# Kernel optimization log

Measured on AMD Instinct MI355X. Metric: run time of the kernel, lower is better.

Reference implementation:

```python
import jax, jax.numpy as jnp
import numpy as np

N_NODES = 100000
DEG = 16
N_EDGES = N_NODES * DEG
D_IN = 128
D_OUT = 128


def setup_inputs() -> dict:
    key = jax.random.key(0)
    k1, k2, k3 = jax.random.split(key, 3)
    X = jax.random.normal(k1, (N_NODES, D_IN), dtype=jnp.float32)
    weights = jax.random.normal(k2, (D_IN, D_OUT), dtype=jnp.float32) * (1.0 / np.sqrt(D_OUT))
    # fixed-degree CSR: row i owns edges [i*DEG, (i+1)*DEG)
    row_pointers = (jnp.arange(N_NODES + 1, dtype=jnp.int32) * DEG)
    column_index = jax.random.randint(k3, (N_EDGES,), 0, N_NODES, dtype=jnp.int32)
    # TC-GNN kernel-scheduling metadata (no effect on math)
    blockPartition = jnp.zeros((N_NODES // DEG,), dtype=jnp.int32)
    edgeToColumn = jnp.zeros((N_EDGES,), dtype=jnp.int32)
    edgeToRow = jnp.zeros((N_EDGES,), dtype=jnp.int32)
    return {"X": X, "weights": weights, "row_pointers": row_pointers,
            "column_index": column_index, "blockPartition": blockPartition,
            "edgeToColumn": edgeToColumn, "edgeToRow": edgeToRow}


def _csr_spmm(feat, row_pointers, column_index):
    # out[i] = sum_{e in row i} feat[column_index[e]]  (unweighted SpMM)
    n = row_pointers.shape[0] - 1
    e = column_index.shape[0]
    # map each edge to its source row via searchsorted on the CSR pointer array
    row_ids = jnp.searchsorted(row_pointers, jnp.arange(e, dtype=row_pointers.dtype), side='right') - 1
    gathered = feat[column_index]  # [E, D]
    return jax.ops.segment_sum(gathered, row_ids, num_segments=n)


def reference(X, weights, row_pointers, column_index, blockPartition, edgeToColumn, edgeToRow):
    X_prime = jnp.matmul(X, weights)                      # [N, D_OUT] dense GEMM
    return _csr_spmm(X_prime, row_pointers, column_index)  # [N, D_OUT] neighbor sum
```

## Files before the change

### kernel.cpp

```cpp
#include <hip/hip_runtime.h>
#include <hip/hip_bf16.h>

#define N_NODES 100000
#define DEG 16
#define D 128

typedef __bf16 bf16x8 __attribute__((ext_vector_type(8)));
typedef float f32x4 __attribute__((ext_vector_type(4)));

__device__ __forceinline__ ushort f32_to_bf16u(float f) {
  unsigned u = __float_as_uint(f);
  u = (u + 0x7fffu + ((u >> 16) & 1u)) >> 16;
  return (ushort)u;
}

__device__ __forceinline__ int swz(int row, int k) {
  return (row << 7) + (k ^ ((row & 7) << 3));
}

__global__ void k_convW(const float* __restrict__ W, ushort* __restrict__ Wt) {
  const int t = threadIdx.x;
  for (int j = 0; j < 64; ++j) {
    int pos = (j << 8) + t;
    int k = pos >> 7, n = pos & 127;
    Wt[swz(n, k)] = f32_to_bf16u(W[pos]);
  }
}

__global__ __launch_bounds__(256, 2) void k_gemm(const float* __restrict__ X,
                                                 const ushort* __restrict__ Wt,
                                                 ushort* __restrict__ Xp) {
  __shared__ __align__(16) ushort As[128 * 128];
  __shared__ __align__(16) ushort Ws[128 * 128];
  const int tid = threadIdx.x;
  const int row0 = blockIdx.x << 7;

  {
    const uint4* src = (const uint4*)Wt;
    uint4* dst = (uint4*)Ws;
#pragma unroll
    for (int j = 0; j < 8; ++j) dst[(j << 8) + tid] = src[(j << 8) + tid];
  }
#pragma unroll
  for (int j = 0; j < 16; ++j) {
    int pos = (j << 8) + tid;
    int r = pos >> 5;
    int c4 = (pos & 31) << 2;
    int grow = row0 + r;
    float4 v = make_float4(0.f, 0.f, 0.f, 0.f);
    if (grow < N_NODES) v = *(const float4*)(X + grow * D + c4);
    ushort4 b;
    b.x = f32_to_bf16u(v.x); b.y = f32_to_bf16u(v.y);
    b.z = f32_to_bf16u(v.z); b.w = f32_to_bf16u(v.w);
    *(ushort4*)(As + swz(r, c4)) = b;
  }
  __syncthreads();

  const int wave = tid >> 6;
  const int lane = tid & 63;
  const int lhi = lane >> 4;
  const int llo = lane & 15;

  f32x4 acc[2][8];
#pragma unroll
  for (int m = 0; m < 2; ++m)
#pragma unroll
    for (int n = 0; n < 8; ++n)
      acc[m][n] = (f32x4){0.f, 0.f, 0.f, 0.f};

#pragma unroll
  for (int t = 0; t < 4; ++t) {
    const int k0 = (t << 5) + (lhi << 3);
    bf16x8 a[2], b[8];
#pragma unroll
    for (int m = 0; m < 2; ++m) {
      int r = (wave << 5) + (m << 4) + llo;
      a[m] = *(const bf16x8*)(As + swz(r, k0));
    }
#pragma unroll
    for (int n = 0; n < 8; ++n) {
      int cc = (n << 4) + llo;
      b[n] = *(const bf16x8*)(Ws + swz(cc, k0));
    }
#pragma unroll
    for (int m = 0; m < 2; ++m)
#pragma unroll
      for (int n = 0; n < 8; ++n)
        acc[m][n] = __builtin_amdgcn_mfma_f32_16x16x32_bf16(a[m], b[n], acc[m][n], 0, 0, 0);
  }

#pragma unroll
  for (int m = 0; m < 2; ++m) {
    int rbase = row0 + (wave << 5) + (m << 4) + (lhi << 2);
#pragma unroll
    for (int n = 0; n < 8; ++n) {
      int col = (n << 4) + llo;
#pragma unroll
      for (int r = 0; r < 4; ++r) {
        int grow = rbase + r;
        if (grow < N_NODES) Xp[grow * D + col] = f32_to_bf16u(acc[m][n][r]);
      }
    }
  }
}

__global__ __launch_bounds__(256) void k_spmm(const ushort* __restrict__ Xp,
                                              const int* __restrict__ ci,
                                              float* __restrict__ out) {
  const int wave = threadIdx.x >> 6;
  const int lane = threadIdx.x & 63;
  const int row = (blockIdx.x << 2) + wave;
  if (row >= N_NODES) return;

  int idx = 0;
  if (lane < DEG) idx = ci[row * DEG + lane];

  float ax = 0.f, ay = 0.f;
#pragma unroll
  for (int e = 0; e < DEG; ++e) {
    int col = __shfl(idx, e);
    unsigned v = *(const unsigned*)(Xp + col * D + (lane << 1));
    ax += __uint_as_float(v << 16);
    ay += __uint_as_float(v & 0xffff0000u);
  }
  *(float2*)(out + row * D + (lane << 1)) = make_float2(ax, ay);
}

extern "C" void kernel_launch(void* const* d_in, const int* in_sizes, int n_in,
                              void* d_out, int out_size, void* d_ws, size_t ws_size,
                              hipStream_t stream) {
  const float* X = (const float*)d_in[0];
  const float* W = (const float*)d_in[1];
  const int* ci = (const int*)d_in[3];

  ushort* Wt = (ushort*)d_ws;
  ushort* Xp = (ushort*)d_ws + 128 * 128;
  float* out = (float*)d_out;

  k_convW<<<1, 256, 0, stream>>>(W, Wt);
  k_gemm<<<(N_NODES + 127) / 128, 256, 0, stream>>>(X, Wt, Xp);
  k_spmm<<<N_NODES / 4, 256, 0, stream>>>(Xp, ci, out);
}
```

Before: 95.72 us.

## Feed GEMM A operand from registers and permute Xp layout for vector stores

The GEMM now loads X rows straight into registers and converts them to bf16 fragments in place, dropping the shared-memory A tile and its barrier traffic. It also writes Xp with a column permutation, so each lane stores a packed 16-byte vector instead of scalar halves. The SpMM kernel issues all 16 neighbour gathers before accumulating, uses nontemporal loads and stores for the index and output streams, and undoes the permutation when writing the output. The cost is that output writes become scattered scalar stores, and register pressure in the GEMM rises.

New measurement: 90.58 us. 1.06x faster.

```diff
diff --git a/kernel.cpp b/kernel.cpp
--- a/kernel.cpp
+++ b/kernel.cpp
@@ -8,10 +8,10 @@
 typedef __bf16 bf16x8 __attribute__((ext_vector_type(8)));
 typedef float f32x4 __attribute__((ext_vector_type(4)));
 
-__device__ __forceinline__ ushort f32_to_bf16u(float f) {
-  unsigned u = __float_as_uint(f);
-  u = (u + 0x7fffu + ((u >> 16) & 1u)) >> 16;
-  return (ushort)u;
+__device__ __forceinline__ unsigned pk2(float a, float b) {
+  union { __bf16 h[2]; unsigned u; } x;
+  x.h[0] = (__bf16)a; x.h[1] = (__bf16)b;
+  return x.u;
 }
 
 __device__ __forceinline__ int swz(int row, int k) {
@@ -23,17 +23,22 @@
   for (int j = 0; j < 64; ++j) {
     int pos = (j << 8) + t;
     int k = pos >> 7, n = pos & 127;
-    Wt[swz(n, k)] = f32_to_bf16u(W[pos]);
+    union { __bf16 h; ushort u; } c;
+    c.h = (__bf16)W[pos];
+    Wt[swz(n, k)] = c.u;
   }
 }
 
 __global__ __launch_bounds__(256, 2) void k_gemm(const float* __restrict__ X,
                                                  const ushort* __restrict__ Wt,
                                                  ushort* __restrict__ Xp) {
-  __shared__ __align__(16) ushort As[128 * 128];
   __shared__ __align__(16) ushort Ws[128 * 128];
   const int tid = threadIdx.x;
   const int row0 = blockIdx.x << 7;
+  const int wave = tid >> 6;
+  const int lane = tid & 63;
+  const int lhi = lane >> 4;
+  const int llo = lane & 15;
 
   {
     const uint4* src = (const uint4*)Wt;
@@ -41,25 +46,20 @@
 #pragma unroll
     for (int j = 0; j < 8; ++j) dst[(j << 8) + tid] = src[(j << 8) + tid];
   }
+
+  float4 xa[2][4][2];
 #pragma unroll
-  for (int j = 0; j < 16; ++j) {
-    int pos = (j << 8) + tid;
-    int r = pos >> 5;
-    int c4 = (pos & 31) << 2;
-    int grow = row0 + r;
-    float4 v = make_float4(0.f, 0.f, 0.f, 0.f);
-    if (grow < N_NODES) v = *(const float4*)(X + grow * D + c4);
-    ushort4 b;
-    b.x = f32_to_bf16u(v.x); b.y = f32_to_bf16u(v.y);
-    b.z = f32_to_bf16u(v.z); b.w = f32_to_bf16u(v.w);
-    *(ushort4*)(As + swz(r, c4)) = b;
+  for (int m = 0; m < 2; ++m) {
+    int row = row0 + (wave << 5) + (m << 4) + llo;
+    const float* rp = X + row * D + (lhi << 3);
+    bool ok = row < N_NODES;
+#pragma unroll
+    for (int t = 0; t < 4; ++t) {
+      xa[m][t][0] = ok ? *(const float4*)(rp + (t << 5)) : make_float4(0.f, 0.f, 0.f, 0.f);
+      xa[m][t][1] = ok ? *(const float4*)(rp + (t << 5) + 4) : make_float4(0.f, 0.f, 0.f, 0.f);
+    }
   }
   __syncthreads();
-
-  const int wave = tid >> 6;
-  const int lane = tid & 63;
-  const int lhi = lane >> 4;
-  const int llo = lane & 15;
 
   f32x4 acc[2][8];
 #pragma unroll
@@ -74,14 +74,15 @@
     bf16x8 a[2], b[8];
 #pragma unroll
     for (int m = 0; m < 2; ++m) {
-      int r = (wave << 5) + (m << 4) + llo;
-      a[m] = *(const bf16x8*)(As + swz(r, k0));
+      float4 p = xa[m][t][0], q = xa[m][t][1];
+      bf16x8 v;
+      v[0] = (__bf16)p.x; v[1] = (__bf16)p.y; v[2] = (__bf16)p.z; v[3] = (__bf16)p.w;
+      v[4] = (__bf16)q.x; v[5] = (__bf16)q.y; v[6] = (__bf16)q.z; v[7] = (__bf16)q.w;
+      a[m] = v;
     }
 #pragma unroll
-    for (int n = 0; n < 8; ++n) {
-      int cc = (n << 4) + llo;
-      b[n] = *(const bf16x8*)(Ws + swz(cc, k0));
-    }
+    for (int n = 0; n < 8; ++n)
+      b[n] = *(const bf16x8*)(Ws + swz((n << 4) + llo, k0));
 #pragma unroll
     for (int m = 0; m < 2; ++m)
 #pragma unroll
@@ -91,14 +92,16 @@
 
 #pragma unroll
   for (int m = 0; m < 2; ++m) {
-    int rbase = row0 + (wave << 5) + (m << 4) + (lhi << 2);
 #pragma unroll
-    for (int n = 0; n < 8; ++n) {
-      int col = (n << 4) + llo;
-#pragma unroll
-      for (int r = 0; r < 4; ++r) {
-        int grow = rbase + r;
-        if (grow < N_NODES) Xp[grow * D + col] = f32_to_bf16u(acc[m][n][r]);
+    for (int r = 0; r < 4; ++r) {
+      int row = row0 + (wave << 5) + (m << 4) + (lhi << 2) + r;
+      if (row < N_NODES) {
+        uint4 v;
+        v.x = pk2(acc[m][0][r], acc[m][1][r]);
+        v.y = pk2(acc[m][2][r], acc[m][3][r]);
+        v.z = pk2(acc[m][4][r], acc[m][5][r]);
+        v.w = pk2(acc[m][6][r], acc[m][7][r]);
+        *(uint4*)(Xp + row * D + (llo << 3)) = v;
       }
     }
   }
@@ -113,17 +116,25 @@
   if (row >= N_NODES) return;
 
   int idx = 0;
-  if (lane < DEG) idx = ci[row * DEG + lane];
+  if (lane < DEG) idx = __builtin_nontemporal_load(ci + row * DEG + lane);
+
+  unsigned v[16];
+#pragma unroll
+  for (int e = 0; e < DEG; ++e) {
+    int col = __shfl(idx, e);
+    v[e] = *(const unsigned*)(Xp + col * D + (lane << 1));
+  }
 
   float ax = 0.f, ay = 0.f;
 #pragma unroll
   for (int e = 0; e < DEG; ++e) {
-    int col = __shfl(idx, e);
-    unsigned v = *(const unsigned*)(Xp + col * D + (lane << 1));
-    ax += __uint_as_float(v << 16);
-    ay += __uint_as_float(v & 0xffff0000u);
+    ax += __uint_as_float(v[e] << 16);
+    ay += __uint_as_float(v[e] & 0xffff0000u);
   }
-  *(float2*)(out + row * D + (lane << 1)) = make_float2(ax, ay);
+
+  const int c0 = (((lane << 1) & 7) << 4) + (lane >> 2);
+  __builtin_nontemporal_store(ax, out + row * D + c0);
+  __builtin_nontemporal_store(ay, out + row * D + c0 + 16);
 }
 
 extern "C" void kernel_launch(void* const* d_in, const int* in_sizes, int n_in,
```
